# Performance work log

Hardware: AMD Instinct MI355X
Metric: run time of the kernel (lower is better)

The kernel has to match this reference:

```python
import jax, jax.numpy as jnp
import numpy as np

L, B, E, H = 512, 64, 512, 1024

def setup_inputs() -> dict:
    key = jax.random.key(0)
    ks = jax.random.split(key, 10)
    scale = 1.0 / np.sqrt(E + H)  # ~torch Linear init scale
    inp = {
        "x": jax.random.normal(ks[0], (L, B, E), dtype=jnp.float32),
        "c": jnp.zeros((B, H), dtype=jnp.float32),
        "h": jnp.zeros((B, H), dtype=jnp.float32),
    }
    names = ["Wf", "bf", "Wi", "bi", "Wg", "bg", "Wo", "bo"]
    for idx, name in enumerate(names):
        k = ks[idx + 1]
        if name.startswith("W"):
            inp[name] = jax.random.normal(k, (E + H, H), dtype=jnp.float32) * scale
        else:
            inp[name] = jax.random.normal(k, (H,), dtype=jnp.float32) * scale
    return inp


def reference(x, c, h, Wf, bf, Wi, bi, Wg, bg, Wo, bo):
    # Fuse the 4 gate projections into one GEMM: same math since all 4 gates
    # consume the identical concat([x_t, h_{t-1}]) input.
    W = jnp.concatenate([Wf, Wi, Wg, Wo], axis=1)  # (E+H, 4H)
    b = jnp.concatenate([bf, bi, bg, bo])          # (4H,)

    def step(carry, x_t):
        c_prev, h_prev = carry
        xh = jnp.concatenate([x_t, h_prev], axis=-1)       # (B, E+H)
        z = xh @ W + b                                     # (B, 4H)
        f_t, i_t, g_t, o_t = jnp.split(z, 4, axis=-1)
        f_t = jax.nn.sigmoid(f_t)
        i_t = jax.nn.sigmoid(i_t)
        g_t = jnp.tanh(g_t)
        o_t = jax.nn.sigmoid(o_t)
        c_t = c_prev * f_t + i_t * g_t
        h_t = o_t * jnp.tanh(c_t)
        return (c_t, h_t), (c_t, h_t)

    (_, _), (c_full, h_full) = jax.lax.scan(step, (c, h), x)
    return c_full, h_full
```

## Files before the change

kernel.cpp:

```cpp
#include <hip/hip_runtime.h>

typedef unsigned int u32;
typedef unsigned short u16;
using u32x4 = __attribute__((ext_vector_type(4))) u32;
using f16x8 = __attribute__((ext_vector_type(8))) _Float16;
using f32x4 = __attribute__((ext_vector_type(4))) float;

#define LT 512
#define BNB 64
#define ED 512
#define HD 1024
#define OUT_HALF_BYTES ((size_t)LT * BNB * HD * 4)

#define WXP_OFF  ((size_t)0)
#define WHP_OFF  ((size_t)(4u << 20))
#define BIAS_OFF ((size_t)(12u << 20))
#define HSTG_OFF ((size_t)((12u << 20) + (16u << 10)))

__device__ __forceinline__ u16 f2h(float f) {
  _Float16 h = (_Float16)f;
  return __builtin_bit_cast(u16, h);
}
__device__ __forceinline__ float h2f(u16 s) {
  return (float)__builtin_bit_cast(_Float16, s);
}
__device__ __forceinline__ u32 pk2(float a, float b) {
  return (u32)f2h(a) | ((u32)f2h(b) << 16);
}
__device__ __forceinline__ void glds16(const void* g, void* l) {
  using GP = const __attribute__((address_space(1))) u32*;
  using SP = __attribute__((address_space(3))) u32*;
  __builtin_amdgcn_global_load_lds((GP)g, (SP)l, 16, 0, 0);
}
__device__ __forceinline__ f32x4 mfma_f16(f16x8 a, f16x8 b, f32x4 c) {
  return __builtin_amdgcn_mfma_f32_16x16x32_f16(a, b, c, 0, 0, 0);
}
__device__ __forceinline__ float sigm(float x) { return 1.0f / (1.0f + __expf(-x)); }
__device__ __forceinline__ float tanh_(float x) { return 2.0f / (1.0f + __expf(-2.0f * x)) - 1.0f; }

__device__ __forceinline__ u32x4 ldg16_cc(const void* p) {
  u32x4 r;
  asm volatile("global_load_dwordx4 %0, %1, off sc0 sc1" : "=v"(r) : "v"(p) : "memory");
  return r;
}
__device__ __forceinline__ void stg_u32_cc(void* p, u32 v) {
  asm volatile("global_store_dword %0, %1, off sc0 sc1" ::"v"(p), "v"(v) : "memory");
}
__device__ __forceinline__ u32 ldg_u16_plain(const void* p) {
  u32 r;
  asm volatile("global_load_ushort %0, %1, off" : "=v"(r) : "v"(p) : "memory");
  return r;
}
__device__ __forceinline__ void waitv0() { asm volatile("s_waitcnt vmcnt(0)" ::: "memory"); }

__device__ __forceinline__ f16x8 unpk(u32x4 lo, u32x4 hi) {
  u32x4 w;
  w[0] = (lo[0] & 0xFFFFu) | (lo[1] << 16);
  w[1] = (lo[2] & 0xFFFFu) | (lo[3] << 16);
  w[2] = (hi[0] & 0xFFFFu) | (hi[1] << 16);
  w[3] = (hi[2] & 0xFFFFu) | (hi[3] << 16);
  return __builtin_bit_cast(f16x8, w);
}


__global__ void pack_wx(const float* __restrict__ Wf, const float* __restrict__ Wi,
                        const float* __restrict__ Wg, const float* __restrict__ Wo,
                        u32x4* __restrict__ dst) {
  const int id = blockIdx.x * 256 + threadIdx.x;
  const int lane = id & 63;
  const int row = id >> 6;
  const int ntile = row >> 7;
  const int rem = row & 127;
  const int kt = rem >> 3;
  const int fn = rem & 7;
  const int np = (ntile << 7) + (fn << 4) + (lane & 15);
  const int g = (np >> 4) & 3;
  const int jfull = ((np >> 6) << 4) + (np & 15);
  const int k0 = (kt << 5) + ((lane >> 4) << 3);
  const float* W = (g == 0) ? Wf : (g == 1) ? Wi : (g == 2) ? Wg : Wo;
  const float* s = W + (size_t)k0 * HD + jfull;
  u16 h[8];
#pragma unroll
  for (int i = 0; i < 8; ++i) h[i] = f2h(s[(size_t)i * HD]);
  u32x4 v;
  v[0] = (u32)h[0] | ((u32)h[1] << 16);
  v[1] = (u32)h[2] | ((u32)h[3] << 16);
  v[2] = (u32)h[4] | ((u32)h[5] << 16);
  v[3] = (u32)h[6] | ((u32)h[7] << 16);
  dst[id] = v;
}

__global__ void pack_wh(const float* __restrict__ Wf, const float* __restrict__ Wi,
                        const float* __restrict__ Wg, const float* __restrict__ Wo,
                        u32x4* __restrict__ dst) {
  const int id = blockIdx.x * 256 + threadIdx.x;
  const int lane = id & 63;
  const int row = id >> 6;
  const int cg = row >> 7;
  const int rem = row & 127;
  const int w = rem >> 5;
  const int g = (rem >> 3) & 3;
  const int kk = rem & 7;
  const int k = ED + (w << 8) + (kk << 5) + ((lane >> 4) << 3);
  const int j = (cg << 4) + (lane & 15);
  const float* W = (g == 0) ? Wf : (g == 1) ? Wi : (g == 2) ? Wg : Wo;
  const float* s = W + (size_t)k * HD + j;
  u16 h[8];
#pragma unroll
  for (int i = 0; i < 8; ++i) h[i] = f2h(s[(size_t)i * HD]);
  u32x4 v;
  v[0] = (u32)h[0] | ((u32)h[1] << 16);
  v[1] = (u32)h[2] | ((u32)h[3] << 16);
  v[2] = (u32)h[4] | ((u32)h[5] << 16);
  v[3] = (u32)h[6] | ((u32)h[7] << 16);
  dst[id] = v;
}

__global__ void pack_bias(const float* __restrict__ bf, const float* __restrict__ bi,
                          const float* __restrict__ bg, const float* __restrict__ bo,
                          float* __restrict__ dst) {
  const int id = blockIdx.x * 256 + threadIdx.x;
  const int g = (id >> 4) & 3;
  const int jfull = ((id >> 6) << 4) + (id & 15);
  const float* B = (g == 0) ? bf : (g == 1) ? bi : (g == 2) ? bg : bo;
  dst[id] = B[jfull];
}


__global__ __launch_bounds__(256) void zx_gemm(const float* __restrict__ x,
                                               const u32x4* __restrict__ wxp,
                                               const float* __restrict__ biasp,
                                               char* __restrict__ outb) {
  __shared__ u32x4 Ab[512];
  __shared__ u32x4 Bb[512];
  const int bid = blockIdx.x;
  const int ntile = bid & 31;
  const int mtile = bid >> 5;
  const int tid = threadIdx.x;
  const int lane = tid & 63;
  const int wid = tid >> 6;
  const int wm = wid & 1;
  const int wn = wid >> 1;
  const int m0 = mtile << 7;

  const f32x4 fz = {0.f, 0.f, 0.f, 0.f};
  f32x4 acc[4][4];
#pragma unroll
  for (int i = 0; i < 4; ++i)
#pragma unroll
    for (int j = 0; j < 4; ++j) acc[i][j] = fz;

  for (int kt = 0; kt < 16; ++kt) {
#pragma unroll
    for (int r = 0; r < 2; ++r) {
      const int c = tid + (r << 8);
      const int fl = c & 63;
      const int fmg = c >> 6;
      const int row = m0 + (fmg << 4) + (fl & 15);
      const int kc = (kt << 5) + ((fl >> 4) << 3);
      const float* s = x + (size_t)row * ED + kc;
      const float4 p0 = *(const float4*)s;
      const float4 p1 = *(const float4*)(s + 4);
      u32x4 v;
      v[0] = pk2(p0.x, p0.y);
      v[1] = pk2(p0.z, p0.w);
      v[2] = pk2(p1.x, p1.y);
      v[3] = pk2(p1.z, p1.w);
      Ab[c] = v;
    }
    {
      const u32x4* bsrc = wxp + (((size_t)(ntile << 4) + kt) << 9);
#pragma unroll
      for (int r = 0; r < 2; ++r) {
        const int cb = (wid << 6) + (r << 8);
        glds16((const void*)(bsrc + cb + lane), (void*)&Bb[cb]);
      }
    }
    __syncthreads();
    f16x8 afr[4], bfr[4];
#pragma unroll
    for (int f = 0; f < 4; ++f) afr[f] = __builtin_bit_cast(f16x8, Ab[((wm * 4 + f) << 6) + lane]);
#pragma unroll
    for (int f = 0; f < 4; ++f) bfr[f] = __builtin_bit_cast(f16x8, Bb[((wn * 4 + f) << 6) + lane]);
#pragma unroll
    for (int fm = 0; fm < 4; ++fm)
#pragma unroll
      for (int fn = 0; fn < 4; ++fn) acc[fm][fn] = mfma_f16(afr[fm], bfr[fn], acc[fm][fn]);
    __syncthreads();
  }

  char* const cb_ = outb;
  char* const hb_ = outb + OUT_HALF_BYTES;
  const int r0 = (lane >> 4) << 2;
#pragma unroll
  for (int fn = 0; fn < 4; ++fn) {
    const int np = (ntile << 7) + (wn << 6) + (fn << 4) + (lane & 15);
    const float bv = biasp[np];
    const int gg = (np >> 4) & 3;
    const int cg = np >> 6;
    const int jj = np & 15;
    char* const outHalf = (gg < 2) ? cb_ : hb_;
    const size_t coloff = (size_t)(cg << 6) + ((gg & 1) << 5) + (jj << 1);
#pragma unroll
    for (int fm = 0; fm < 4; ++fm) {
#pragma unroll
      for (int r = 0; r < 4; ++r) {
        const int m = m0 + (wm << 6) + (fm << 4) + r0 + r;
        *(u16*)(outHalf + (size_t)m * 4096 + coloff) = f2h(acc[fm][fn][r] + bv);
      }
    }
  }
}


__global__ __launch_bounds__(256, 1) void lstm_rec(const float* __restrict__ c0,
                                                   const float* __restrict__ h0,
                                                   const u32x4* __restrict__ whp, char* outb,
                                                   u32* hstg) {
  __shared__ float zb[4][4][16][17];
  const int bid = blockIdx.x;
  const int mslab = bid & 3;
  const int cgp = bid >> 2;
  const int tid = threadIdx.x;
  const int lane = tid & 63;
  const int wid = tid >> 6;
  const int b_loc = tid >> 4;
  const int j_loc = tid & 15;
  const int b = (mslab << 4) + b_loc;
  const int jf = (cgp << 4) + j_loc;

  f16x8 wreg[4][8];
  {
    const u32x4* wb = whp + (((size_t)(cgp * 4 + wid)) << 11);
#pragma unroll
    for (int g = 0; g < 4; ++g)
#pragma unroll
      for (int kk = 0; kk < 8; ++kk)
        wreg[g][kk] = __builtin_bit_cast(f16x8, wb[((g << 3) + kk) * 64 + lane]);
  }
  float creg = c0[(b << 10) + jf];
  stg_u32_cc(hstg + (b << 10) + jf, (u32)f2h(h0[(b << 10) + jf]));

  char* const cb_ = outb;
  char* const hb_ = outb + OUT_HALF_BYTES;

  u32 xf16, xi16, xg16, xo16;
  {
    const size_t rowb = ((size_t)b) << 12;
    const char* crow = cb_ + rowb + (cgp << 6);
    const char* hrow = hb_ + rowb + (cgp << 6);
    xf16 = ldg_u16_plain(crow + (j_loc << 1));
    xi16 = ldg_u16_plain(crow + 32 + (j_loc << 1));
    xg16 = ldg_u16_plain(hrow + (j_loc << 1));
    xo16 = ldg_u16_plain(hrow + 32 + (j_loc << 1));
  }

  const u32 aoff = (u32)((((mslab << 4) + (lane & 15)) << 10) + (wid << 8) + ((lane >> 4) << 3));

  const f32x4 fz = {0.f, 0.f, 0.f, 0.f};
#pragma unroll 1
  for (int t = 0; t < LT; ++t) {
    const u32* ab = hstg + (((u32)t & 1) << 16) + aoff;
    const u32 gtag = (u32)t << 16;
    u32x4 v[16];
    for (;;) {
#pragma unroll
      for (int kk = 0; kk < 8; ++kk) {
        v[2 * kk] = ldg16_cc(ab + (kk << 5));
        v[2 * kk + 1] = ldg16_cc(ab + (kk << 5) + 4);
      }
      waitv0();
      u32 acm = 0;
#pragma unroll
      for (int i = 0; i < 16; ++i)
        acm |= (v[i][0] ^ gtag) | (v[i][1] ^ gtag) | (v[i][2] ^ gtag) | (v[i][3] ^ gtag);
      if (__all(acm < 0x10000u)) break;
      __builtin_amdgcn_s_sleep(1);
    }

    f32x4 a0 = fz, a1 = fz, a2 = fz, a3 = fz;
#pragma unroll
    for (int kk = 0; kk < 8; ++kk) {
      const f16x8 av = unpk(v[2 * kk], v[2 * kk + 1]);
      a0 = mfma_f16(av, wreg[0][kk], a0);
      a1 = mfma_f16(av, wreg[1][kk], a1);
      a2 = mfma_f16(av, wreg[2][kk], a2);
      a3 = mfma_f16(av, wreg[3][kk], a3);
    }
    {
      const int rr = (lane >> 4) << 2;
      const int cc = lane & 15;
#pragma unroll
      for (int r = 0; r < 4; ++r) {
        zb[wid][0][rr + r][cc] = a0[r];
        zb[wid][1][rr + r][cc] = a1[r];
        zb[wid][2][rr + r][cc] = a2[r];
        zb[wid][3][rr + r][cc] = a3[r];
      }
    }
    __syncthreads();

    float zf = h2f((u16)xf16), zi = h2f((u16)xi16);
    float zg = h2f((u16)xg16), zo = h2f((u16)xo16);
#pragma unroll
    for (int w = 0; w < 4; ++w) {
      zf += zb[w][0][b_loc][j_loc];
      zi += zb[w][1][b_loc][j_loc];
      zg += zb[w][2][b_loc][j_loc];
      zo += zb[w][3][b_loc][j_loc];
    }
    __syncthreads();

    const float fg = sigm(zf), ig = sigm(zi), gg = tanh_(zg), og = sigm(zo);
    creg = creg * fg + ig * gg;
    const float hv = og * tanh_(creg);

    stg_u32_cc(hstg + ((((u32)(t + 1)) & 1) << 16) + (b << 10) + jf,
               (((u32)(t + 1)) << 16) | (u32)f2h(hv));

    const size_t rowoff = ((size_t)((t << 6) + b)) << 12;
    *(float*)(cb_ + rowoff + ((size_t)jf << 2)) = creg;
    *(float*)(hb_ + rowoff + ((size_t)jf << 2)) = hv;

    {
      const int tn = (t + 1 < LT) ? t + 1 : t;
      const size_t rown = ((size_t)((tn << 6) + b)) << 12;
      const char* crow = cb_ + rown + (cgp << 6);
      const char* hrow = hb_ + rown + (cgp << 6);
      xf16 = ldg_u16_plain(crow + (j_loc << 1));
      xi16 = ldg_u16_plain(crow + 32 + (j_loc << 1));
      xg16 = ldg_u16_plain(hrow + (j_loc << 1));
      xo16 = ldg_u16_plain(hrow + 32 + (j_loc << 1));
    }
  }
}

extern "C" void kernel_launch(void* const* d_in, const int* in_sizes, int n_in, void* d_out,
                              int out_size, void* d_ws, size_t ws_size, hipStream_t stream) {
  const float* x = (const float*)d_in[0];
  const float* c0 = (const float*)d_in[1];
  const float* h0 = (const float*)d_in[2];
  const float* Wf = (const float*)d_in[3];
  const float* bf = (const float*)d_in[4];
  const float* Wi = (const float*)d_in[5];
  const float* bi = (const float*)d_in[6];
  const float* Wg = (const float*)d_in[7];
  const float* bg = (const float*)d_in[8];
  const float* Wo = (const float*)d_in[9];
  const float* bo = (const float*)d_in[10];

  char* ws = (char*)d_ws;
  u32x4* wxp = (u32x4*)(ws + WXP_OFF);
  u32x4* whp = (u32x4*)(ws + WHP_OFF);
  float* bp = (float*)(ws + BIAS_OFF);
  u32* hstg = (u32*)(ws + HSTG_OFF);

  pack_wx<<<1024, 256, 0, stream>>>(Wf, Wi, Wg, Wo, wxp);
  pack_wh<<<2048, 256, 0, stream>>>(Wf, Wi, Wg, Wo, whp);
  pack_bias<<<16, 256, 0, stream>>>(bf, bi, bg, bo, bp);
  zx_gemm<<<8192, 256, 0, stream>>>(x, wxp, bp, (char*)d_out);
  lstm_rec<<<256, 256, 0, stream>>>(c0, h0, whp, (char*)d_out, hstg);
}
```

Before: 2.843 ms.

## Halve recurrent blocks and add per-block flag sync before polling h

The recurrent kernel now runs on 128 blocks instead of 256. Each block handles 32 hidden columns, with twice as many weight fragments held in registers and two cell states per thread. Each block publishes a per-step progress flag, and consumers spin on the flags of the 32 peer blocks in their batch slab before loading the tagged h staging buffer, with the sleep in the retry loop removed. The goal is to cut the number of participants in the cross-block barrier and the repeated wide polling loads, at the cost of more MFMA work per block, higher register pressure (64 f16x8 weight registers), and an extra flag round trip each step.

```diff
diff --git a/kernel.cpp b/kernel.cpp
--- a/kernel.cpp
+++ b/kernel.cpp
@@ -16,6 +16,7 @@
 #define WHP_OFF  ((size_t)(4u << 20))
 #define BIAS_OFF ((size_t)(12u << 20))
 #define HSTG_OFF ((size_t)((12u << 20) + (16u << 10)))
+#define FLAG_OFF ((size_t)((12u << 20) + (16u << 10) + (512u << 10)))
 
 __device__ __forceinline__ u16 f2h(float f) {
   _Float16 h = (_Float16)f;
@@ -41,6 +42,12 @@
 __device__ __forceinline__ u32x4 ldg16_cc(const void* p) {
   u32x4 r;
   asm volatile("global_load_dwordx4 %0, %1, off sc0 sc1" : "=v"(r) : "v"(p) : "memory");
+  return r;
+}
+__device__ __forceinline__ u32 ld_flag_cc(const void* p) {
+  u32 r;
+  asm volatile("global_load_dword %0, %1, off sc0 sc1\n\ts_waitcnt vmcnt(0)"
+               : "=v"(r) : "v"(p) : "memory");
   return r;
 }
 __device__ __forceinline__ void stg_u32_cc(void* p, u32 v) {
@@ -96,15 +103,16 @@
   const int id = blockIdx.x * 256 + threadIdx.x;
   const int lane = id & 63;
   const int row = id >> 6;
-  const int cg = row >> 7;
-  const int rem = row & 127;
-  const int w = rem >> 5;
-  const int g = (rem >> 3) & 3;
-  const int kk = rem & 7;
+  const int kk = row & 7;
+  const int w = (row >> 3) & 3;
+  const int nt = (row >> 5) & 7;
+  const int cq = row >> 8;
+  const int np = (cq << 7) + (nt << 4) + (lane & 15);
+  const int g = (np >> 4) & 3;
+  const int jfull = ((np >> 6) << 4) + (np & 15);
   const int k = ED + (w << 8) + (kk << 5) + ((lane >> 4) << 3);
-  const int j = (cg << 4) + (lane & 15);
   const float* W = (g == 0) ? Wf : (g == 1) ? Wi : (g == 2) ? Wg : Wo;
-  const float* s = W + (size_t)k * HD + j;
+  const float* s = W + (size_t)k * HD + jfull;
   u16 h[8];
 #pragma unroll
   for (int i = 0; i < 8; ++i) h[i] = f2h(s[(size_t)i * HD]);
@@ -116,14 +124,15 @@
   dst[id] = v;
 }
 
-__global__ void pack_bias(const float* __restrict__ bf, const float* __restrict__ bi,
-                          const float* __restrict__ bg, const float* __restrict__ bo,
-                          float* __restrict__ dst) {
+__global__ void pack_bias_flags(const float* __restrict__ bf, const float* __restrict__ bi,
+                                const float* __restrict__ bg, const float* __restrict__ bo,
+                                float* __restrict__ dst, int* __restrict__ flags) {
   const int id = blockIdx.x * 256 + threadIdx.x;
   const int g = (id >> 4) & 3;
   const int jfull = ((id >> 6) << 4) + (id & 15);
   const float* B = (g == 0) ? bf : (g == 1) ? bi : (g == 2) ? bg : bo;
   dst[id] = B[jfull];
+  flags[id] = 0;
 }
 
 
@@ -216,50 +225,56 @@
 __global__ __launch_bounds__(256, 1) void lstm_rec(const float* __restrict__ c0,
                                                    const float* __restrict__ h0,
                                                    const u32x4* __restrict__ whp, char* outb,
-                                                   u32* hstg) {
-  __shared__ float zb[4][4][16][17];
+                                                   u32* hstg, int* flags) {
+  __shared__ float zb[4][8][16][17];
   const int bid = blockIdx.x;
   const int mslab = bid & 3;
-  const int cgp = bid >> 2;
+  const int cq = bid >> 2;
   const int tid = threadIdx.x;
   const int lane = tid & 63;
   const int wid = tid >> 6;
   const int b_loc = tid >> 4;
   const int j_loc = tid & 15;
   const int b = (mslab << 4) + b_loc;
-  const int jf = (cgp << 4) + j_loc;
-
-  f16x8 wreg[4][8];
-  {
-    const u32x4* wb = whp + (((size_t)(cgp * 4 + wid)) << 11);
-#pragma unroll
-    for (int g = 0; g < 4; ++g)
-#pragma unroll
-      for (int kk = 0; kk < 8; ++kk)
-        wreg[g][kk] = __builtin_bit_cast(f16x8, wb[((g << 3) + kk) * 64 + lane]);
-  }
-  float creg = c0[(b << 10) + jf];
-  stg_u32_cc(hstg + (b << 10) + jf, (u32)f2h(h0[(b << 10) + jf]));
+  const int col0 = (cq << 5) + j_loc;
+
+  f16x8 wreg[8][8];
+#pragma unroll
+  for (int nt = 0; nt < 8; ++nt)
+#pragma unroll
+    for (int kk = 0; kk < 8; ++kk)
+      wreg[nt][kk] = __builtin_bit_cast(
+          f16x8, whp[((size_t)((cq << 8) + (nt << 5) + (wid << 3) + kk) << 6) + lane]);
+
+  float creg0 = c0[(b << 10) + col0];
+  float creg1 = c0[(b << 10) + col0 + 16];
+  stg_u32_cc(hstg + (b << 10) + col0, (u32)f2h(h0[(b << 10) + col0]));
+  stg_u32_cc(hstg + (b << 10) + col0 + 16, (u32)f2h(h0[(b << 10) + col0 + 16]));
 
   char* const cb_ = outb;
   char* const hb_ = outb + OUT_HALF_BYTES;
 
-  u32 xf16, xi16, xg16, xo16;
+  u32 zx0[4], zx1[4];
   {
     const size_t rowb = ((size_t)b) << 12;
-    const char* crow = cb_ + rowb + (cgp << 6);
-    const char* hrow = hb_ + rowb + (cgp << 6);
-    xf16 = ldg_u16_plain(crow + (j_loc << 1));
-    xi16 = ldg_u16_plain(crow + 32 + (j_loc << 1));
-    xg16 = ldg_u16_plain(hrow + (j_loc << 1));
-    xo16 = ldg_u16_plain(hrow + 32 + (j_loc << 1));
+#pragma unroll
+    for (int g = 0; g < 4; ++g) {
+      const char* half = (g < 2) ? cb_ : hb_;
+      zx0[g] = ldg_u16_plain(half + rowb + (cq << 7) + ((g & 1) << 5) + (j_loc << 1));
+      zx1[g] = ldg_u16_plain(half + rowb + (cq << 7) + 64 + ((g & 1) << 5) + (j_loc << 1));
+    }
   }
+  __syncthreads();
+  if (tid == 0) stg_u32_cc(flags + (((mslab << 5) + cq) << 2), 1u);
 
   const u32 aoff = (u32)((((mslab << 4) + (lane & 15)) << 10) + (wid << 8) + ((lane >> 4) << 3));
+  const int* const pf = flags + (((mslab << 5) + (lane & 31)) << 2);
 
   const f32x4 fz = {0.f, 0.f, 0.f, 0.f};
 #pragma unroll 1
   for (int t = 0; t < LT; ++t) {
+    while ((int)ld_flag_cc(pf) < t + 1) {}
+
     const u32* ab = hstg + (((u32)t & 1) << 16) + aoff;
     const u32 gtag = (u32)t << 16;
     u32x4 v[16];
@@ -275,62 +290,77 @@
       for (int i = 0; i < 16; ++i)
         acm |= (v[i][0] ^ gtag) | (v[i][1] ^ gtag) | (v[i][2] ^ gtag) | (v[i][3] ^ gtag);
       if (__all(acm < 0x10000u)) break;
-      __builtin_amdgcn_s_sleep(1);
-    }
-
-    f32x4 a0 = fz, a1 = fz, a2 = fz, a3 = fz;
+    }
+
+    f32x4 acc[8];
+#pragma unroll
+    for (int nt = 0; nt < 8; ++nt) acc[nt] = fz;
 #pragma unroll
     for (int kk = 0; kk < 8; ++kk) {
       const f16x8 av = unpk(v[2 * kk], v[2 * kk + 1]);
-      a0 = mfma_f16(av, wreg[0][kk], a0);
-      a1 = mfma_f16(av, wreg[1][kk], a1);
-      a2 = mfma_f16(av, wreg[2][kk], a2);
-      a3 = mfma_f16(av, wreg[3][kk], a3);
+#pragma unroll
+      for (int nt = 0; nt < 8; ++nt) acc[nt] = mfma_f16(av, wreg[nt][kk], acc[nt]);
     }
     {
       const int rr = (lane >> 4) << 2;
       const int cc = lane & 15;
 #pragma unroll
-      for (int r = 0; r < 4; ++r) {
-        zb[wid][0][rr + r][cc] = a0[r];
-        zb[wid][1][rr + r][cc] = a1[r];
-        zb[wid][2][rr + r][cc] = a2[r];
-        zb[wid][3][rr + r][cc] = a3[r];
-      }
+      for (int nt = 0; nt < 8; ++nt)
+#pragma unroll
+        for (int r = 0; r < 4; ++r) zb[wid][nt][rr + r][cc] = acc[nt][r];
     }
     __syncthreads();
 
-    float zf = h2f((u16)xf16), zi = h2f((u16)xi16);
-    float zg = h2f((u16)xg16), zo = h2f((u16)xo16);
-#pragma unroll
-    for (int w = 0; w < 4; ++w) {
-      zf += zb[w][0][b_loc][j_loc];
-      zi += zb[w][1][b_loc][j_loc];
-      zg += zb[w][2][b_loc][j_loc];
-      zo += zb[w][3][b_loc][j_loc];
-    }
+    float hv0, hv1;
+    {
+      float z[4];
+#pragma unroll
+      for (int g = 0; g < 4; ++g) {
+        float s = h2f((u16)zx0[g]);
+#pragma unroll
+        for (int w = 0; w < 4; ++w) s += zb[w][g][b_loc][j_loc];
+        z[g] = s;
+      }
+      const float fg = sigm(z[0]), ig = sigm(z[1]), gg = tanh_(z[2]), og = sigm(z[3]);
+      creg0 = creg0 * fg + ig * gg;
+      hv0 = og * tanh_(creg0);
+    }
+    {
+      float z[4];
+#pragma unroll
+      for (int g = 0; g < 4; ++g) {
+        float s = h2f((u16)zx1[g]);
+#pragma unroll
+        for (int w = 0; w < 4; ++w) s += zb[w][4 + g][b_loc][j_loc];
+        z[g] = s;
+      }
+      const float fg = sigm(z[0]), ig = sigm(z[1]), gg = tanh_(z[2]), og = sigm(z[3]);
+      creg1 = creg1 * fg + ig * gg;
+      hv1 = og * tanh_(creg1);
+    }
+
+    const u32 ntag = ((u32)(t + 1)) << 16;
+    u32* hdst = hstg + ((((u32)(t + 1)) & 1) << 16) + (b << 10) + col0;
+    stg_u32_cc(hdst, ntag | (u32)f2h(hv0));
+    stg_u32_cc(hdst + 16, ntag | (u32)f2h(hv1));
     __syncthreads();
-
-    const float fg = sigm(zf), ig = sigm(zi), gg = tanh_(zg), og = sigm(zo);
-    creg = creg * fg + ig * gg;
-    const float hv = og * tanh_(creg);
-
-    stg_u32_cc(hstg + ((((u32)(t + 1)) & 1) << 16) + (b << 10) + jf,
-               (((u32)(t + 1)) << 16) | (u32)f2h(hv));
+    if (tid == 0) stg_u32_cc(flags + (((mslab << 5) + cq) << 2), (u32)(t + 2));
 
     const size_t rowoff = ((size_t)((t << 6) + b)) << 12;
-    *(float*)(cb_ + rowoff + ((size_t)jf << 2)) = creg;
-    *(float*)(hb_ + rowoff + ((size_t)jf << 2)) = hv;
+    *(float*)(cb_ + rowoff + ((size_t)col0 << 2)) = creg0;
+    *(float*)(cb_ + rowoff + ((size_t)(col0 + 16) << 2)) = creg1;
+    *(float*)(hb_ + rowoff + ((size_t)col0 << 2)) = hv0;
+    *(float*)(hb_ + rowoff + ((size_t)(col0 + 16) << 2)) = hv1;
 
     {
       const int tn = (t + 1 < LT) ? t + 1 : t;
       const size_t rown = ((size_t)((tn << 6) + b)) << 12;
-      const char* crow = cb_ + rown + (cgp << 6);
-      const char* hrow = hb_ + rown + (cgp << 6);
-      xf16 = ldg_u16_plain(crow + (j_loc << 1));
-      xi16 = ldg_u16_plain(crow + 32 + (j_loc << 1));
-      xg16 = ldg_u16_plain(hrow + (j_loc << 1));
-      xo16 = ldg_u16_plain(hrow + 32 + (j_loc << 1));
+#pragma unroll
+      for (int g = 0; g < 4; ++g) {
+        const char* half = (g < 2) ? cb_ : hb_;
+        zx0[g] = ldg_u16_plain(half + rown + (cq << 7) + ((g & 1) << 5) + (j_loc << 1));
+        zx1[g] = ldg_u16_plain(half + rown + (cq << 7) + 64 + ((g & 1) << 5) + (j_loc << 1));
+      }
     }
   }
 }
@@ -354,10 +384,11 @@
   u32x4* whp = (u32x4*)(ws + WHP_OFF);
   float* bp = (float*)(ws + BIAS_OFF);
   u32* hstg = (u32*)(ws + HSTG_OFF);
+  int* flags = (int*)(ws + FLAG_OFF);
 
   pack_wx<<<1024, 256, 0, stream>>>(Wf, Wi, Wg, Wo, wxp);
   pack_wh<<<2048, 256, 0, stream>>>(Wf, Wi, Wg, Wo, whp);
-  pack_bias<<<16, 256, 0, stream>>>(bf, bi, bg, bo, bp);
+  pack_bias_flags<<<16, 256, 0, stream>>>(bf, bi, bg, bo, bp, flags);
   zx_gemm<<<8192, 256, 0, stream>>>(x, wxp, bp, (char*)d_out);
-  lstm_rec<<<256, 256, 0, stream>>>(c0, h0, whp, (char*)d_out, hstg);
-}
+  lstm_rec<<<128, 256, 0, stream>>>(c0, h0, whp, (char*)d_out, hstg, flags);
+}
```

New measurement: 2.773 ms. -2.5%, faster.
